# Performance work log

Measured on AMD Instinct MI355X. Metric: run time of the kernel, lower is better.

The kernel has to match this reference:

```python
import jax, jax.numpy as jnp
import numpy as np

EPS = 1e-5

def _ln(x, g, b):
    m = jnp.mean(x, -1, keepdims=True)
    v = jnp.mean((x - m) ** 2, -1, keepdims=True)
    return (x - m) * jax.lax.rsqrt(v + EPS) * g + b

def _lstm(x, Wih, Whh, bih, bhh):
    # x: [B, T, D]; torch gate order i, f, g, o; h0 = c0 = 0
    B = x.shape[0]
    H = Whh.shape[1]
    h0 = jnp.zeros((B, H), x.dtype)
    c0 = jnp.zeros((B, H), x.dtype)
    bias = bih + bhh
    def step(carry, xt):
        h, c = carry
        gates = xt @ Wih.T + h @ Whh.T + bias  # [B, 4H]
        i, f, g, o = jnp.split(gates, 4, axis=-1)
        c = jax.nn.sigmoid(f) * c + jax.nn.sigmoid(i) * jnp.tanh(g)
        h = jax.nn.sigmoid(o) * jnp.tanh(c)
        return (h, c), h
    _, hs = jax.lax.scan(step, (h0, c0), jnp.swapaxes(x, 0, 1))
    return jnp.swapaxes(hs, 0, 1)  # [B, T, H]

def setup_inputs() -> dict:
    key = jax.random.key(0)
    ks = jax.random.split(key, 20)
    N, C, F, T = 4, 64, 256, 256
    D, H = 128, 32  # LSTM in/out
    s = 0.05
    inp = {
        "inputs": jax.random.normal(ks[0], (N, C, F, T, 2), jnp.float32),
        "ln1_g": jnp.ones((D,), jnp.float32), "ln1_b": jnp.zeros((D,), jnp.float32),
        "Wih_q": s * jax.random.normal(ks[1], (4 * H, D), jnp.float32),
        "Whh_q": s * jax.random.normal(ks[2], (4 * H, H), jnp.float32),
        "bih_q": s * jax.random.normal(ks[3], (4 * H,), jnp.float32),
        "bhh_q": s * jax.random.normal(ks[4], (4 * H,), jnp.float32),
        "Wih_k": s * jax.random.normal(ks[5], (4 * H, D), jnp.float32),
        "Whh_k": s * jax.random.normal(ks[6], (4 * H, H), jnp.float32),
        "bih_k": s * jax.random.normal(ks[7], (4 * H,), jnp.float32),
        "bhh_k": s * jax.random.normal(ks[8], (4 * H,), jnp.float32),
        "Wih_v": s * jax.random.normal(ks[9], (4 * H, D), jnp.float32),
        "Whh_v": s * jax.random.normal(ks[10], (4 * H, H), jnp.float32),
        "bih_v": s * jax.random.normal(ks[11], (4 * H,), jnp.float32),
        "bhh_v": s * jax.random.normal(ks[12], (4 * H,), jnp.float32),
        "ln2_g": jnp.ones((H,), jnp.float32), "ln2_b": jnp.zeros((H,), jnp.float32),
        "Wr": s * jax.random.normal(ks[13], (C, H // 2), jnp.float32),
        "br": s * jax.random.normal(ks[14], (C,), jnp.float32),
        "Wi": s * jax.random.normal(ks[15], (C, H // 2), jnp.float32),
        "bi": s * jax.random.normal(ks[16], (C,), jnp.float32),
        "ln3_g": jnp.ones((C,), jnp.float32), "ln3_b": jnp.zeros((C,), jnp.float32),
        "prelu_a": jnp.full((1,), 0.25, jnp.float32),
    }
    return inp

def reference(inputs, ln1_g, ln1_b,
              Wih_q, Whh_q, bih_q, bhh_q,
              Wih_k, Whh_k, bih_k, bhh_k,
              Wih_v, Whh_v, bih_v, bhh_v,
              ln2_g, ln2_b, Wr, br, Wi, bi,
              ln3_g, ln3_b, prelu_a):
    N, C, F, T, ri = inputs.shape
    # [N,C,F,T,2] -> [N*F, T, C, 2] -> concat real/imag -> [N*F, T, 2C]
    x4 = jnp.transpose(inputs, (0, 2, 3, 1, 4)).reshape(N * F, T, C, ri)
    x = jnp.concatenate([x4[..., 0], x4[..., 1]], axis=-1)  # [B, T, 128]
    # Self_Attention_T_RICAT (single head)
    xn = _ln(x, ln1_g, ln1_b)
    q = _lstm(xn, Wih_q, Whh_q, bih_q, bhh_q)  # [B, T, 32]
    k = _lstm(xn, Wih_k, Whh_k, bih_k, bhh_k)
    v = _lstm(xn, Wih_v, Whh_v, bih_v, bhh_v)
    energy = jnp.einsum('btf,bsf->bts', q, k) / 4.0  # / 16**0.5
    mask = jnp.tril(jnp.ones((T, T), x.dtype))
    attn = jax.nn.softmax(energy * mask, axis=-1)  # multiplicative mask, as in source
    wv = jnp.einsum('bts,bsf->btf', attn, v)  # [B, T, 32]
    out = _ln(wv, ln2_g, ln2_b)
    # complex-valued linear fusion
    xr, xi = jnp.split(out, 2, axis=-1)  # [B, T, 16] each
    lr_r = xr @ Wr.T + br
    li_i = xi @ Wi.T + bi
    lr_i = xi @ Wr.T + br
    li_r = xr @ Wi.T + bi
    out_real = (lr_r - li_i).reshape(N, F, T, C).transpose(0, 3, 1, 2)  # [N,C,F,T]
    out_imag = (lr_i + li_r).reshape(N, F, T, C).transpose(0, 3, 1, 2)
    outs = jnp.stack([out_real, out_imag], axis=-1)  # [N,C,F,T,2]
    outs_t = jnp.swapaxes(outs, 1, 4)  # [N,2,F,T,C]
    outs = jnp.swapaxes(_ln(outs_t, ln3_g, ln3_b), 1, 4)
    outs = jnp.where(outs >= 0, outs, prelu_a[0] * outs)  # PReLU (eval mode, dropout=identity)
    return outs + inputs
```

## Files before the change

kernel.cpp:

```cpp
#include <hip/hip_runtime.h>
#include <hip/hip_bf16.h>
#include <stddef.h>


typedef __bf16 bf16x8 __attribute__((ext_vector_type(8)));
typedef float f32x4 __attribute__((ext_vector_type(4)));

__device__ __forceinline__ ushort f2bf(float x) {
    uint u = __builtin_bit_cast(uint, x);
    uint r = (u + 0x7fffu + ((u >> 16) & 1u)) >> 16;
    return (ushort)r;
}

__device__ __forceinline__ float fsig(float x) {
    return __builtin_amdgcn_rcpf(1.f + __expf(-x));
}
__device__ __forceinline__ float ftanh(float x) {
    return 1.f - 2.f * __builtin_amdgcn_rcpf(__expf(2.f * x) + 1.f);
}
__device__ __forceinline__ float wredsum(float v) {
#pragma unroll
    for (int off = 32; off; off >>= 1) v += __shfl_xor(v, off);
    return v;
}
__device__ __forceinline__ float hredsum(float v) {
#pragma unroll
    for (int off = 16; off; off >>= 1) v += __shfl_xor(v, off);
    return v;
}

__global__ __launch_bounds__(256) void k_prep(const float* __restrict__ in,
                                              const float* __restrict__ g1,
                                              const float* __restrict__ b1,
                                              ushort* __restrict__ xn) {
    __shared__ float xl[32][129];
    const int n = blockIdx.z, f = blockIdx.y, t0 = blockIdx.x * 32;
    const int tid = threadIdx.x;
    const int c = tid >> 2, q = tid & 3;
    const float* src = in + ((size_t)(n * 64 + c) * 256 + f) * 512 + t0 * 2 + q * 16;
#pragma unroll
    for (int e = 0; e < 4; ++e) {
        float4 v4 = *(const float4*)(src + e * 4);
        int dt = q * 8 + e * 2;
        xl[dt][c]          = v4.x;
        xl[dt][c + 64]     = v4.y;
        xl[dt + 1][c]      = v4.z;
        xl[dt + 1][c + 64] = v4.w;
    }
    __syncthreads();
    const int lane = tid & 63, w = tid >> 6;
    const int b = n * 256 + f;
#pragma unroll 1
    for (int r = 0; r < 8; ++r) {
        int dt = w * 8 + r;
        float a = xl[dt][lane], bb = xl[dt][lane + 64];
        float s = wredsum(a + bb);
        float mean = s * 0.0078125f;
        float da = a - mean, db = bb - mean;
        float var = wredsum(da * da + db * db) * 0.0078125f;
        float inv = __builtin_amdgcn_rsqf(var + 1e-5f);
        size_t base = ((size_t)b * 256 + (t0 + dt)) * 128;
        xn[base + lane]      = f2bf(da * inv * g1[lane] + b1[lane]);
        xn[base + lane + 64] = f2bf(db * inv * g1[lane + 64] + b1[lane + 64]);
    }
}

__global__ __launch_bounds__(256) void k_gemm(const ushort* __restrict__ xn,
                                              const float* __restrict__ Wq,
                                              const float* __restrict__ Wk,
                                              const float* __restrict__ Wv,
                                              const float* __restrict__ bihq, const float* __restrict__ bhhq,
                                              const float* __restrict__ bihk, const float* __restrict__ bhhk,
                                              const float* __restrict__ bihv, const float* __restrict__ bhhv,
                                              ushort* __restrict__ gx) {
    __shared__ ushort a_lds[128 * 136];
    __shared__ ushort w_lds[64 * 136];
    const int tid = threadIdx.x;
    const int m0 = blockIdx.x * 128;
    const int yb = blockIdx.y;
    const int l = yb >> 1, n0 = (yb & 1) * 64;
    const float* W   = (l == 0) ? Wq   : (l == 1) ? Wk   : Wv;
    const float* bih = (l == 0) ? bihq : (l == 1) ? bihk : bihv;
    const float* bhh = (l == 0) ? bhhq : (l == 1) ? bhhk : bhhv;

#pragma unroll
    for (int p = 0; p < 8; ++p) {
        int idx = p * 256 + tid;
        int r = idx >> 4, c = idx & 15;
        uint4 v = *(const uint4*)(xn + (size_t)(m0 + r) * 128 + c * 8);
        *(uint4*)&a_lds[r * 136 + c * 8] = v;
    }
#pragma unroll
    for (int p = 0; p < 4; ++p) {
        int idx = p * 256 + tid;
        int r = idx >> 4, c = idx & 15;
        const float* wp = W + (size_t)(n0 + r) * 128 + c * 8;
        float4 wa = *(const float4*)wp;
        float4 wb = *(const float4*)(wp + 4);
        union { ushort u[8]; uint4 v; } pk;
        pk.u[0] = f2bf(wa.x); pk.u[1] = f2bf(wa.y); pk.u[2] = f2bf(wa.z); pk.u[3] = f2bf(wa.w);
        pk.u[4] = f2bf(wb.x); pk.u[5] = f2bf(wb.y); pk.u[6] = f2bf(wb.z); pk.u[7] = f2bf(wb.w);
        *(uint4*)&w_lds[r * 136 + c * 8] = pk.v;
    }
    __syncthreads();

    const int w = tid >> 6, lane = tid & 63;
    const int wr = w >> 1, wc = w & 1;
    const int row16 = lane & 15, koct = lane >> 4;

    f32x4 acc[4][2];
#pragma unroll
    for (int mi = 0; mi < 4; ++mi)
#pragma unroll
        for (int ni = 0; ni < 2; ++ni) acc[mi][ni] = (f32x4){0.f, 0.f, 0.f, 0.f};

#pragma unroll
    for (int ki = 0; ki < 4; ++ki) {
        bf16x8 af[4], bfr[2];
#pragma unroll
        for (int mi = 0; mi < 4; ++mi)
            af[mi] = *(const bf16x8*)&a_lds[(wr * 64 + mi * 16 + row16) * 136 + ki * 32 + koct * 8];
#pragma unroll
        for (int ni = 0; ni < 2; ++ni)
            bfr[ni] = *(const bf16x8*)&w_lds[(wc * 32 + ni * 16 + row16) * 136 + ki * 32 + koct * 8];
#pragma unroll
        for (int mi = 0; mi < 4; ++mi)
#pragma unroll
            for (int ni = 0; ni < 2; ++ni)
                acc[mi][ni] = __builtin_amdgcn_mfma_f32_16x16x32_bf16(af[mi], bfr[ni], acc[mi][ni], 0, 0, 0);
    }

    float bs[2];
#pragma unroll
    for (int ni = 0; ni < 2; ++ni) {
        int ncol = n0 + wc * 32 + ni * 16 + row16;
        bs[ni] = bih[ncol] + bhh[ncol];
    }
#pragma unroll
    for (int mi = 0; mi < 4; ++mi)
#pragma unroll
        for (int ni = 0; ni < 2; ++ni) {
            int ncol = n0 + wc * 32 + ni * 16 + row16;
            int pos = ((ncol & 31) << 2) | (ncol >> 5);
#pragma unroll
            for (int q = 0; q < 4; ++q) {
                size_t m = (size_t)m0 + wr * 64 + mi * 16 + koct * 4 + q;
                gx[m * 384 + l * 128 + pos] = f2bf(acc[mi][ni][q] + bs[ni]);
            }
        }
}

__global__ __launch_bounds__(128) void k_lstm(const ushort* __restrict__ gx,
                                              const float* __restrict__ Whq,
                                              const float* __restrict__ Whk,
                                              const float* __restrict__ Whv,
                                              ushort* __restrict__ qkv) {
    __shared__ ushort H[2][16][40];
    const int tid = threadIdx.x, w = tid >> 6, lane = tid & 63;
    const int r16 = lane & 15, koct = lane >> 4;
    const int l = blockIdx.x >> 6, bgrp = blockIdx.x & 63;
    const int b = bgrp * 16 + r16;
    const float* Wh = (l == 0) ? Whq : (l == 1) ? Whk : Whv;
    bf16x8 wf[4];
#pragma unroll
    for (int gidx = 0; gidx < 4; ++gidx) {
        int grow = (gidx * 2 + w) * 16 + r16;
        const float* wp = Wh + (size_t)grow * 32 + koct * 8;
        float4 wa = *(const float4*)wp;
        float4 wb2 = *(const float4*)(wp + 4);
        union { ushort u[8]; bf16x8 v; } pk;
        pk.u[0] = f2bf(wa.x);  pk.u[1] = f2bf(wa.y);  pk.u[2] = f2bf(wa.z);  pk.u[3] = f2bf(wa.w);
        pk.u[4] = f2bf(wb2.x); pk.u[5] = f2bf(wb2.y); pk.u[6] = f2bf(wb2.z); pk.u[7] = f2bf(wb2.w);
        wf[gidx] = pk.v;
    }
    for (int i = tid; i < 640; i += 128) ((ushort*)H[0])[i] = 0;
    __syncthreads();
    const char* gbase = (const char*)gx + (size_t)(b * 256) * 768 + l * 256 + w * 128 + koct * 32;
    uint4 pf[2][2];
#pragma unroll
    for (int tt = 0; tt < 2; ++tt) {
        pf[tt][0] = *(const uint4*)(gbase + (size_t)tt * 768);
        pf[tt][1] = *(const uint4*)(gbase + (size_t)tt * 768 + 16);
    }
    float c4[4] = {0.f, 0.f, 0.f, 0.f};
    const int j0 = w * 16 + koct * 4;
    ushort* outp = qkv + ((size_t)(l * 1024 + b)) * 8192 + j0;
#pragma unroll 2
    for (int t = 0; t < 256; ++t) {
        const int rb = t & 1, wbuf = (t + 1) & 1;
        bf16x8 hf = *(const bf16x8*)&H[rb][r16][koct * 8];
        uint4 ca = pf[t & 1][0], cb = pf[t & 1][1];
        {
            int tn = (t + 2 < 256) ? t + 2 : 255;
            pf[t & 1][0] = *(const uint4*)(gbase + (size_t)tn * 768);
            pf[t & 1][1] = *(const uint4*)(gbase + (size_t)tn * 768 + 16);
        }
        uint eu[8] = {ca.x, ca.y, ca.z, ca.w, cb.x, cb.y, cb.z, cb.w};
        f32x4 acc[4];
#pragma unroll
        for (int gidx = 0; gidx < 4; ++gidx) {
#pragma unroll
            for (int q = 0; q < 4; ++q) {
                int e = 4 * q + gidx;
                uint u = eu[e >> 1];
                uint bfv = (e & 1) ? (u & 0xffff0000u) : (u << 16);
                acc[gidx][q] = __builtin_bit_cast(float, bfv);
            }
        }
#pragma unroll
        for (int gidx = 0; gidx < 4; ++gidx)
            acc[gidx] = __builtin_amdgcn_mfma_f32_16x16x32_bf16(wf[gidx], hf, acc[gidx], 0, 0, 0);
        ushort hu[4];
#pragma unroll
        for (int q = 0; q < 4; ++q) {
            float gi = acc[0][q], gf = acc[1][q], gg = acc[2][q], go = acc[3][q];
            float cN = fsig(gf) * c4[q] + fsig(gi) * ftanh(gg);
            c4[q] = cN;
            hu[q] = f2bf(fsig(go) * ftanh(cN));
        }
        uint2 hp = make_uint2((uint)hu[0] | ((uint)hu[1] << 16),
                              (uint)hu[2] | ((uint)hu[3] << 16));
        *(uint2*)&H[wbuf][r16][j0] = hp;
        *(uint2*)(outp + (size_t)t * 32) = hp;
        __syncthreads();
    }
}

__global__ __launch_bounds__(256) void k_attn(const ushort* __restrict__ qkvb,
                                              float* __restrict__ wvout) {
    __shared__ ushort k_sw[256 * 32];
    __shared__ ushort vt_sw[32 * 256];
    __shared__ ushort p_sw[4][16 * 256];
    const int tid = threadIdx.x, w = tid >> 6, lane = tid & 63;
    const int b = blockIdx.x;
    const ushort* qb = qkvb + (size_t)b * 8192;
    const ushort* kb = qkvb + 8388608 + (size_t)b * 8192;
    const ushort* vb = qkvb + 16777216 + (size_t)b * 8192;
#pragma unroll
    for (int p = 0; p < 4; ++p) {
        int idx = p * 256 + tid;
        int s = idx >> 2, cc = idx & 3;
        uint4 kv = *(const uint4*)(kb + s * 32 + cc * 8);
        int cK = cc ^ ((s >> 1) & 3);
        *(uint4*)&k_sw[s * 32 + cK * 8] = kv;
        uint4 vv = *(const uint4*)(vb + s * 32 + cc * 8);
        union { uint4 v; ushort u[8]; } un; un.v = vv;
#pragma unroll
        for (int e = 0; e < 8; ++e) {
            int row = cc * 8 + e;
            vt_sw[row * 256 + (((s >> 3) ^ (row & 7)) << 3) + (s & 7)] = un.u[e];
        }
    }
    __syncthreads();
    const int r16 = lane & 15, koct = lane >> 4;
    ushort* pw = p_sw[w];
    bf16x8 qf[4];
#pragma unroll
    for (int i = 0; i < 4; ++i) {
        int t = (w * 4 + i) * 16 + r16;
        qf[i] = *(const bf16x8*)(qb + t * 32 + koct * 8);
    }
#pragma unroll 1
    for (int i = 0; i < 4; ++i) {
        const int tb = (w * 4 + i) * 16;
        f32x4 acc[16];
#pragma unroll
        for (int st = 0; st < 16; ++st) acc[st] = (f32x4){0.f, 0.f, 0.f, 0.f};
#pragma unroll
        for (int st = 0; st < 16; ++st) {
            int s = st * 16 + r16;
            int cK = koct ^ ((s >> 1) & 3);
            bf16x8 kf = *(const bf16x8*)&k_sw[s * 32 + cK * 8];
            acc[st] = __builtin_amdgcn_mfma_f32_16x16x32_bf16(qf[i], kf, acc[st], 0, 0, 0);
        }
        float mx[4] = {-1e30f, -1e30f, -1e30f, -1e30f};
#pragma unroll
        for (int st = 0; st < 16; ++st) {
            int s = st * 16 + r16;
#pragma unroll
            for (int q = 0; q < 4; ++q) {
                int t = tb + koct * 4 + q;
                float v = (s <= t) ? acc[st][q] * 0.25f : 0.f;
                acc[st][q] = v;
                mx[q] = fmaxf(mx[q], v);
            }
        }
#pragma unroll
        for (int off = 1; off < 16; off <<= 1)
#pragma unroll
            for (int q = 0; q < 4; ++q) mx[q] = fmaxf(mx[q], __shfl_xor(mx[q], off));
        float sm[4] = {0.f, 0.f, 0.f, 0.f};
#pragma unroll
        for (int st = 0; st < 16; ++st)
#pragma unroll
            for (int q = 0; q < 4; ++q) {
                float p = __expf(acc[st][q] - mx[q]);
                acc[st][q] = p; sm[q] += p;
            }
#pragma unroll
        for (int off = 1; off < 16; off <<= 1)
#pragma unroll
            for (int q = 0; q < 4; ++q) sm[q] += __shfl_xor(sm[q], off);
        float rs[4];
#pragma unroll
        for (int q = 0; q < 4; ++q) rs[q] = __builtin_amdgcn_rcpf(sm[q]);
#pragma unroll
        for (int st = 0; st < 16; ++st) {
            int schunk = st * 2 + (r16 >> 3), sl = r16 & 7;
#pragma unroll
            for (int q = 0; q < 4; ++q) {
                int tl = koct * 4 + q;
                pw[tl * 256 + ((schunk ^ (tl & 7)) << 3) + sl] = f2bf(acc[st][q] * rs[q]);
            }
        }
        __asm__ volatile("s_waitcnt lgkmcnt(0)" ::: "memory");
        f32x4 oa[2];
        oa[0] = (f32x4){0.f, 0.f, 0.f, 0.f};
        oa[1] = (f32x4){0.f, 0.f, 0.f, 0.f};
#pragma unroll
        for (int ks = 0; ks < 8; ++ks) {
            int kc = ks * 4 + koct;
            bf16x8 pa = *(const bf16x8*)&pw[r16 * 256 + ((kc ^ (r16 & 7)) << 3)];
#pragma unroll
            for (int n = 0; n < 2; ++n) {
                int row = n * 16 + r16;
                bf16x8 vf = *(const bf16x8*)&vt_sw[row * 256 + ((kc ^ (row & 7)) << 3)];
                oa[n] = __builtin_amdgcn_mfma_f32_16x16x32_bf16(pa, vf, oa[n], 0, 0, 0);
            }
        }
#pragma unroll
        for (int n = 0; n < 2; ++n)
#pragma unroll
            for (int q = 0; q < 4; ++q)
                wvout[((size_t)b * 256 + tb + koct * 4 + q) * 32 + n * 16 + r16] = oa[n][q];
    }
}

__global__ __launch_bounds__(256) void k_post(const float* __restrict__ wv,
                                              const float* __restrict__ in,
                                              const float* __restrict__ g2,
                                              const float* __restrict__ b2,
                                              const float* __restrict__ Wr,
                                              const float* __restrict__ br,
                                              const float* __restrict__ Wi,
                                              const float* __restrict__ bi,
                                              const float* __restrict__ g3,
                                              const float* __restrict__ b3,
                                              const float* __restrict__ pa,
                                              float* __restrict__ outp) {
    __shared__ float xv[32][33];
    __shared__ float wr_l[64][17], wi_l[64][17];
    __shared__ float out_s[64][65];
    const int tid = threadIdx.x;
    const int n = blockIdx.z, f = blockIdx.y, t0 = blockIdx.x * 32;
    const int b = n * 256 + f;
    for (int idx = tid; idx < 1024; idx += 256) {
        int dt = idx >> 5, j = idx & 31;
        xv[dt][j] = wv[((size_t)b * 256 + t0 + dt) * 32 + j];
        int cc = idx >> 4, jjj = idx & 15;
        wr_l[cc][jjj] = Wr[idx];
        wi_l[cc][jjj] = Wi[idx];
    }
    __syncthreads();
    const int lane = tid & 63, w = tid >> 6;
#pragma unroll 1
    for (int r = 0; r < 4; ++r) {
        int dt = w * 8 + r * 2 + (lane >> 5);
        int j = lane & 31;
        float v = xv[dt][j];
        float mean = hredsum(v) * 0.03125f;
        float d = v - mean;
        float var = hredsum(d * d) * 0.03125f;
        float inv = __builtin_amdgcn_rsqf(var + 1e-5f);
        xv[dt][j] = d * inv * g2[j] + b2[j];
    }
    __syncthreads();
    const int c = lane;
    const float g3c = g3[c], b3c = b3[c];
    const float bd = br[c] - bi[c], bsum = br[c] + bi[c];
    const float alpha = pa[0];
#pragma unroll 1
    for (int r = 0; r < 8; ++r) {
        int dt = w * 8 + r;
        float re = 0.f, im = 0.f;
#pragma unroll
        for (int j = 0; j < 16; ++j) {
            float xr = xv[dt][j], xi2 = xv[dt][16 + j];
            float wrv = wr_l[c][j], wiv = wi_l[c][j];
            re += xr * wrv; re -= xi2 * wiv;
            im += xi2 * wrv; im += xr * wiv;
        }
        re += bd; im += bsum;
        float mR = wredsum(re) * 0.015625f;
        float dR = re - mR;
        float vR = wredsum(dR * dR) * 0.015625f;
        float nR = dR * __builtin_amdgcn_rsqf(vR + 1e-5f) * g3c + b3c;
        nR = (nR >= 0.f) ? nR : alpha * nR;
        float mI = wredsum(im) * 0.015625f;
        float dI = im - mI;
        float vI = wredsum(dI * dI) * 0.015625f;
        float nI = dI * __builtin_amdgcn_rsqf(vI + 1e-5f) * g3c + b3c;
        nI = (nI >= 0.f) ? nI : alpha * nI;
        out_s[c][dt * 2]     = nR;
        out_s[c][dt * 2 + 1] = nI;
    }
    __syncthreads();
    const int cc = tid >> 2, q = tid & 3;
    size_t base = ((size_t)(n * 64 + cc) * 256 + f) * 512 + t0 * 2 + q * 16;
#pragma unroll
    for (int e = 0; e < 4; ++e) {
        float4 iv = *(const float4*)(in + base + e * 4);
        int k0 = q * 16 + e * 4;
        float4 ov;
        ov.x = out_s[cc][k0]     + iv.x;
        ov.y = out_s[cc][k0 + 1] + iv.y;
        ov.z = out_s[cc][k0 + 2] + iv.z;
        ov.w = out_s[cc][k0 + 3] + iv.w;
        *(float4*)(outp + base + e * 4) = ov;
    }
}

extern "C" void kernel_launch(void* const* d_in, const int* in_sizes, int n_in,
                              void* d_out, int out_size, void* d_ws, size_t ws_size,
                              hipStream_t stream) {
    const float* in   = (const float*)d_in[0];
    const float* g1   = (const float*)d_in[1];
    const float* b1   = (const float*)d_in[2];
    const float* Wq   = (const float*)d_in[3];
    const float* Whq  = (const float*)d_in[4];
    const float* bihq = (const float*)d_in[5];
    const float* bhhq = (const float*)d_in[6];
    const float* Wk   = (const float*)d_in[7];
    const float* Whk  = (const float*)d_in[8];
    const float* bihk = (const float*)d_in[9];
    const float* bhhk = (const float*)d_in[10];
    const float* Wv   = (const float*)d_in[11];
    const float* Whv  = (const float*)d_in[12];
    const float* bihv = (const float*)d_in[13];
    const float* bhhv = (const float*)d_in[14];
    const float* g2   = (const float*)d_in[15];
    const float* b2   = (const float*)d_in[16];
    const float* Wr   = (const float*)d_in[17];
    const float* br   = (const float*)d_in[18];
    const float* Wi   = (const float*)d_in[19];
    const float* bi   = (const float*)d_in[20];
    const float* g3   = (const float*)d_in[21];
    const float* b3   = (const float*)d_in[22];
    const float* pa   = (const float*)d_in[23];
    float* outp = (float*)d_out;

    ushort* gxb  = (ushort*)d_ws;
    ushort* xnb  = (ushort*)((char*)d_ws + 201326592);
    ushort* qkvb = (ushort*)((char*)d_ws + 268435456);
    float*  wvb  = (float*)((char*)d_ws + 318767104);

    k_prep<<<dim3(8, 256, 4), dim3(256), 0, stream>>>(in, g1, b1, xnb);
    k_gemm<<<dim3(2048, 6), dim3(256), 0, stream>>>(xnb, Wq, Wk, Wv,
                                                    bihq, bhhq, bihk, bhhk, bihv, bhhv, gxb);
    k_lstm<<<dim3(192), dim3(128), 0, stream>>>(gxb, Whq, Whk, Whv, qkvb);
    k_attn<<<dim3(1024), dim3(256), 0, stream>>>(qkvb, wvb);
    k_post<<<dim3(8, 256, 4), dim3(256), 0, stream>>>(wvb, in, g2, b2,
                                                      Wr, br, Wi, bi, g3, b3, pa, outp);
}
```

Measured before the change: 573.8 us.

## Run each LSTM batch group in a single wave and fuse all three GEMM projections per block

The LSTM kernel now uses one 64-lane wave per 16-sequence group. Each lane computes all four gates for its hidden units, which removes the cross-wave __syncthreads at every time step and leaves only a wave-local LDS round trip. The gate columns written by the GEMM are permuted so each lane's i/f/g/o values come out of the MFMA together. The input GEMM now loops over the q/k/v weights inside one block, so the xn tile is loaded once instead of six times. The cost is fewer waves in flight during the serial recurrence (192 single-wave blocks) and twice the MFMA work per wave on each step.

```diff
diff --git a/kernel.cpp b/kernel.cpp
--- a/kernel.cpp
+++ b/kernel.cpp
@@ -74,156 +74,156 @@
                                               const float* __restrict__ bihv, const float* __restrict__ bhhv,
                                               ushort* __restrict__ gx) {
     __shared__ ushort a_lds[128 * 136];
-    __shared__ ushort w_lds[64 * 136];
+    __shared__ ushort w_lds[128 * 136];
     const int tid = threadIdx.x;
     const int m0 = blockIdx.x * 128;
-    const int yb = blockIdx.y;
-    const int l = yb >> 1, n0 = (yb & 1) * 64;
-    const float* W   = (l == 0) ? Wq   : (l == 1) ? Wk   : Wv;
-    const float* bih = (l == 0) ? bihq : (l == 1) ? bihk : bihv;
-    const float* bhh = (l == 0) ? bhhq : (l == 1) ? bhhk : bhhv;
 
 #pragma unroll
     for (int p = 0; p < 8; ++p) {
         int idx = p * 256 + tid;
         int r = idx >> 4, c = idx & 15;
-        uint4 v = *(const uint4*)(xn + (size_t)(m0 + r) * 128 + c * 8);
-        *(uint4*)&a_lds[r * 136 + c * 8] = v;
-    }
-#pragma unroll
-    for (int p = 0; p < 4; ++p) {
-        int idx = p * 256 + tid;
-        int r = idx >> 4, c = idx & 15;
-        const float* wp = W + (size_t)(n0 + r) * 128 + c * 8;
-        float4 wa = *(const float4*)wp;
-        float4 wb = *(const float4*)(wp + 4);
-        union { ushort u[8]; uint4 v; } pk;
-        pk.u[0] = f2bf(wa.x); pk.u[1] = f2bf(wa.y); pk.u[2] = f2bf(wa.z); pk.u[3] = f2bf(wa.w);
-        pk.u[4] = f2bf(wb.x); pk.u[5] = f2bf(wb.y); pk.u[6] = f2bf(wb.z); pk.u[7] = f2bf(wb.w);
-        *(uint4*)&w_lds[r * 136 + c * 8] = pk.v;
-    }
-    __syncthreads();
+        *(uint4*)&a_lds[r * 136 + c * 8] =
+            *(const uint4*)(xn + (size_t)(m0 + r) * 128 + c * 8);
+    }
 
     const int w = tid >> 6, lane = tid & 63;
     const int wr = w >> 1, wc = w & 1;
     const int row16 = lane & 15, koct = lane >> 4;
 
-    f32x4 acc[4][2];
-#pragma unroll
-    for (int mi = 0; mi < 4; ++mi)
-#pragma unroll
-        for (int ni = 0; ni < 2; ++ni) acc[mi][ni] = (f32x4){0.f, 0.f, 0.f, 0.f};
-
-#pragma unroll
-    for (int ki = 0; ki < 4; ++ki) {
-        bf16x8 af[4], bfr[2];
+#pragma unroll 1
+    for (int l = 0; l < 3; ++l) {
+        const float* W   = (l == 0) ? Wq   : (l == 1) ? Wk   : Wv;
+        const float* bih = (l == 0) ? bihq : (l == 1) ? bihk : bihv;
+        const float* bhh = (l == 0) ? bhhq : (l == 1) ? bhhk : bhhv;
+        __syncthreads();
+#pragma unroll
+        for (int p = 0; p < 8; ++p) {
+            int idx = p * 256 + tid;
+            int r = idx >> 4, c = idx & 15;
+            const float* wp = W + (size_t)r * 128 + c * 8;
+            float4 wa = *(const float4*)wp;
+            float4 wb = *(const float4*)(wp + 4);
+            union { ushort u[8]; uint4 v; } pk;
+            pk.u[0] = f2bf(wa.x); pk.u[1] = f2bf(wa.y); pk.u[2] = f2bf(wa.z); pk.u[3] = f2bf(wa.w);
+            pk.u[4] = f2bf(wb.x); pk.u[5] = f2bf(wb.y); pk.u[6] = f2bf(wb.z); pk.u[7] = f2bf(wb.w);
+            *(uint4*)&w_lds[r * 136 + c * 8] = pk.v;
+        }
+        __syncthreads();
+
+        f32x4 acc[4][4];
 #pragma unroll
         for (int mi = 0; mi < 4; ++mi)
-            af[mi] = *(const bf16x8*)&a_lds[(wr * 64 + mi * 16 + row16) * 136 + ki * 32 + koct * 8];
-#pragma unroll
-        for (int ni = 0; ni < 2; ++ni)
-            bfr[ni] = *(const bf16x8*)&w_lds[(wc * 32 + ni * 16 + row16) * 136 + ki * 32 + koct * 8];
-#pragma unroll
-        for (int mi = 0; mi < 4; ++mi)
-#pragma unroll
-            for (int ni = 0; ni < 2; ++ni)
-                acc[mi][ni] = __builtin_amdgcn_mfma_f32_16x16x32_bf16(af[mi], bfr[ni], acc[mi][ni], 0, 0, 0);
-    }
-
-    float bs[2];
-#pragma unroll
-    for (int ni = 0; ni < 2; ++ni) {
-        int ncol = n0 + wc * 32 + ni * 16 + row16;
-        bs[ni] = bih[ncol] + bhh[ncol];
-    }
-#pragma unroll
-    for (int mi = 0; mi < 4; ++mi)
-#pragma unroll
-        for (int ni = 0; ni < 2; ++ni) {
-            int ncol = n0 + wc * 32 + ni * 16 + row16;
-            int pos = ((ncol & 31) << 2) | (ncol >> 5);
-#pragma unroll
-            for (int q = 0; q < 4; ++q) {
-                size_t m = (size_t)m0 + wr * 64 + mi * 16 + koct * 4 + q;
-                gx[m * 384 + l * 128 + pos] = f2bf(acc[mi][ni][q] + bs[ni]);
-            }
-        }
-}
-
-__global__ __launch_bounds__(128) void k_lstm(const ushort* __restrict__ gx,
-                                              const float* __restrict__ Whq,
-                                              const float* __restrict__ Whk,
-                                              const float* __restrict__ Whv,
-                                              ushort* __restrict__ qkv) {
-    __shared__ ushort H[2][16][40];
-    const int tid = threadIdx.x, w = tid >> 6, lane = tid & 63;
+#pragma unroll
+            for (int ni = 0; ni < 4; ++ni) acc[mi][ni] = (f32x4){0.f, 0.f, 0.f, 0.f};
+
+#pragma unroll
+        for (int ki = 0; ki < 4; ++ki) {
+            bf16x8 af[4], bfr[4];
+#pragma unroll
+            for (int mi = 0; mi < 4; ++mi)
+                af[mi] = *(const bf16x8*)&a_lds[(wr * 64 + mi * 16 + row16) * 136 + ki * 32 + koct * 8];
+#pragma unroll
+            for (int ni = 0; ni < 4; ++ni)
+                bfr[ni] = *(const bf16x8*)&w_lds[(wc * 64 + ni * 16 + row16) * 136 + ki * 32 + koct * 8];
+#pragma unroll
+            for (int mi = 0; mi < 4; ++mi)
+#pragma unroll
+                for (int ni = 0; ni < 4; ++ni)
+                    acc[mi][ni] = __builtin_amdgcn_mfma_f32_16x16x32_bf16(af[mi], bfr[ni], acc[mi][ni], 0, 0, 0);
+        }
+
+#pragma unroll
+        for (int ni = 0; ni < 4; ++ni) {
+            int g = wc * 64 + ni * 16 + row16;
+            float bsv = bih[g] + bhh[g];
+            int j = g & 31, gi = g >> 5;
+            int s = (j & 3) * 32 + (j >> 2) * 4 + gi;
+#pragma unroll
+            for (int mi = 0; mi < 4; ++mi)
+#pragma unroll
+                for (int q = 0; q < 4; ++q) {
+                    size_t m = (size_t)m0 + wr * 64 + mi * 16 + koct * 4 + q;
+                    gx[m * 384 + l * 128 + s] = f2bf(acc[mi][ni][q] + bsv);
+                }
+        }
+    }
+}
+
+__global__ __launch_bounds__(64) void k_lstm(const ushort* __restrict__ gx,
+                                             const float* __restrict__ Whq,
+                                             const float* __restrict__ Whk,
+                                             const float* __restrict__ Whv,
+                                             ushort* __restrict__ qkv) {
+    __shared__ ushort H[16][34];
+    const int lane = threadIdx.x & 63;
     const int r16 = lane & 15, koct = lane >> 4;
     const int l = blockIdx.x >> 6, bgrp = blockIdx.x & 63;
     const int b = bgrp * 16 + r16;
     const float* Wh = (l == 0) ? Whq : (l == 1) ? Whk : Whv;
-    bf16x8 wf[4];
-#pragma unroll
-    for (int gidx = 0; gidx < 4; ++gidx) {
-        int grow = (gidx * 2 + w) * 16 + r16;
-        const float* wp = Wh + (size_t)grow * 32 + koct * 8;
+
+    bf16x8 wf[8];
+#pragma unroll
+    for (int g = 0; g < 8; ++g) {
+        int p = g * 16 + r16;
+        int row = (p & 3) * 32 + (p >> 2);
+        const float* wp = Wh + (size_t)row * 32 + koct * 8;
         float4 wa = *(const float4*)wp;
-        float4 wb2 = *(const float4*)(wp + 4);
+        float4 wb = *(const float4*)(wp + 4);
         union { ushort u[8]; bf16x8 v; } pk;
-        pk.u[0] = f2bf(wa.x);  pk.u[1] = f2bf(wa.y);  pk.u[2] = f2bf(wa.z);  pk.u[3] = f2bf(wa.w);
-        pk.u[4] = f2bf(wb2.x); pk.u[5] = f2bf(wb2.y); pk.u[6] = f2bf(wb2.z); pk.u[7] = f2bf(wb2.w);
-        wf[gidx] = pk.v;
-    }
-    for (int i = tid; i < 640; i += 128) ((ushort*)H[0])[i] = 0;
-    __syncthreads();
-    const char* gbase = (const char*)gx + (size_t)(b * 256) * 768 + l * 256 + w * 128 + koct * 32;
-    uint4 pf[2][2];
-#pragma unroll
-    for (int tt = 0; tt < 2; ++tt) {
-        pf[tt][0] = *(const uint4*)(gbase + (size_t)tt * 768);
-        pf[tt][1] = *(const uint4*)(gbase + (size_t)tt * 768 + 16);
-    }
-    float c4[4] = {0.f, 0.f, 0.f, 0.f};
-    const int j0 = w * 16 + koct * 4;
-    ushort* outp = qkv + ((size_t)(l * 1024 + b)) * 8192 + j0;
+        pk.u[0] = f2bf(wa.x); pk.u[1] = f2bf(wa.y); pk.u[2] = f2bf(wa.z); pk.u[3] = f2bf(wa.w);
+        pk.u[4] = f2bf(wb.x); pk.u[5] = f2bf(wb.y); pk.u[6] = f2bf(wb.z); pk.u[7] = f2bf(wb.w);
+        wf[g] = pk.v;
+    }
+
+    const ushort* gp = gx + (size_t)b * 98304 + l * 128 + koct * 32;
+    uint pf[2][16];
+#pragma unroll
+    for (int tt = 0; tt < 2; ++tt)
+#pragma unroll
+        for (int i = 0; i < 4; ++i)
+            *(uint4*)&pf[tt][i * 4] = *(const uint4*)(gp + (size_t)tt * 384 + i * 8);
+
+    float cst[8] = {0.f, 0.f, 0.f, 0.f, 0.f, 0.f, 0.f, 0.f};
+    uint4 z4 = make_uint4(0, 0, 0, 0);
+    bf16x8 hf = __builtin_bit_cast(bf16x8, z4);
+    ushort* outp = qkv + ((size_t)(l * 1024 + b)) * 8192 + koct * 8;
+
 #pragma unroll 2
     for (int t = 0; t < 256; ++t) {
-        const int rb = t & 1, wbuf = (t + 1) & 1;
-        bf16x8 hf = *(const bf16x8*)&H[rb][r16][koct * 8];
-        uint4 ca = pf[t & 1][0], cb = pf[t & 1][1];
-        {
-            int tn = (t + 2 < 256) ? t + 2 : 255;
-            pf[t & 1][0] = *(const uint4*)(gbase + (size_t)tn * 768);
-            pf[t & 1][1] = *(const uint4*)(gbase + (size_t)tn * 768 + 16);
-        }
-        uint eu[8] = {ca.x, ca.y, ca.z, ca.w, cb.x, cb.y, cb.z, cb.w};
-        f32x4 acc[4];
-#pragma unroll
-        for (int gidx = 0; gidx < 4; ++gidx) {
+        const int sl = t & 1;
+        uint u[16];
+#pragma unroll
+        for (int i = 0; i < 16; ++i) u[i] = pf[sl][i];
+        int tn = (t + 2 < 256) ? t + 2 : 255;
+#pragma unroll
+        for (int i = 0; i < 4; ++i)
+            *(uint4*)&pf[sl][i * 4] = *(const uint4*)(gp + (size_t)tn * 384 + i * 8);
+
+        f32x4 acc[8];
+#pragma unroll
+        for (int g = 0; g < 8; ++g)
 #pragma unroll
             for (int q = 0; q < 4; ++q) {
-                int e = 4 * q + gidx;
-                uint u = eu[e >> 1];
-                uint bfv = (e & 1) ? (u & 0xffff0000u) : (u << 16);
-                acc[gidx][q] = __builtin_bit_cast(float, bfv);
+                int v = g * 4 + q;
+                uint w32 = u[v >> 1];
+                acc[g][q] = __builtin_bit_cast(float, (v & 1) ? (w32 & 0xffff0000u) : (w32 << 16));
             }
-        }
-#pragma unroll
-        for (int gidx = 0; gidx < 4; ++gidx)
-            acc[gidx] = __builtin_amdgcn_mfma_f32_16x16x32_bf16(wf[gidx], hf, acc[gidx], 0, 0, 0);
-        ushort hu[4];
-#pragma unroll
-        for (int q = 0; q < 4; ++q) {
-            float gi = acc[0][q], gf = acc[1][q], gg = acc[2][q], go = acc[3][q];
-            float cN = fsig(gf) * c4[q] + fsig(gi) * ftanh(gg);
-            c4[q] = cN;
-            hu[q] = f2bf(fsig(go) * ftanh(cN));
-        }
-        uint2 hp = make_uint2((uint)hu[0] | ((uint)hu[1] << 16),
-                              (uint)hu[2] | ((uint)hu[3] << 16));
-        *(uint2*)&H[wbuf][r16][j0] = hp;
-        *(uint2*)(outp + (size_t)t * 32) = hp;
-        __syncthreads();
-    }
+#pragma unroll
+        for (int g = 0; g < 8; ++g)
+            acc[g] = __builtin_amdgcn_mfma_f32_16x16x32_bf16(wf[g], hf, acc[g], 0, 0, 0);
+
+        if (t > 0) *(bf16x8*)(outp + (size_t)(t - 1) * 32) = hf;
+
+#pragma unroll
+        for (int g = 0; g < 8; ++g) {
+            float gi = acc[g][0], gf = acc[g][1], gg = acc[g][2], go = acc[g][3];
+            float cN = fsig(gf) * cst[g] + fsig(gi) * ftanh(gg);
+            cst[g] = cN;
+            H[r16][g * 4 + koct] = f2bf(fsig(go) * ftanh(cN));
+        }
+        hf = *(const bf16x8*)&H[r16][koct * 8];
+    }
+    *(bf16x8*)(outp + (size_t)255 * 32) = hf;
 }
 
 __global__ __launch_bounds__(256) void k_attn(const ushort* __restrict__ qkvb,
@@ -455,9 +455,9 @@
     float*  wvb  = (float*)((char*)d_ws + 318767104);
 
     k_prep<<<dim3(8, 256, 4), dim3(256), 0, stream>>>(in, g1, b1, xnb);
-    k_gemm<<<dim3(2048, 6), dim3(256), 0, stream>>>(xnb, Wq, Wk, Wv,
-                                                    bihq, bhhq, bihk, bhhk, bihv, bhhv, gxb);
-    k_lstm<<<dim3(192), dim3(128), 0, stream>>>(gxb, Whq, Whk, Whv, qkvb);
+    k_gemm<<<dim3(2048), dim3(256), 0, stream>>>(xnb, Wq, Wk, Wv,
+                                                 bihq, bhhq, bihk, bhhk, bihv, bhhv, gxb);
+    k_lstm<<<dim3(192), dim3(64), 0, stream>>>(gxb, Whq, Whk, Whv, qkvb);
     k_attn<<<dim3(1024), dim3(256), 0, stream>>>(qkvb, wvb);
     k_post<<<dim3(8, 256, 4), dim3(256), 0, stream>>>(wvb, in, g2, b2,
                                                       Wr, br, Wi, bi, g3, b3, pa, outp);
```

After: 623.1 us. +8.6%, slower.
